# Performance work log

Measured on AMD Instinct MI355X. Metric: run time of the kernel, lower is better.

## Reference

```python
import jax, jax.numpy as jnp
import numpy as np

EMB_DIM = 2048
HIDDEN_DIM = 8192
BATCH = 4
SEQ = 2048


def _kaiming_normal(key, out_f, in_f):
    # kaiming_normal_(mode='fan_in', nonlinearity='relu'): std = sqrt(2 / fan_in)
    std = np.sqrt(2.0 / in_f).astype(np.float32)
    return jax.random.normal(key, (out_f, in_f), dtype=jnp.float32) * std


def setup_inputs() -> dict:
    key = jax.random.key(0)
    kx, k1, k2, k3 = jax.random.split(key, 4)
    x = jax.random.normal(kx, (BATCH, SEQ, EMB_DIM), dtype=jnp.float32)
    w1 = _kaiming_normal(k1, HIDDEN_DIM, EMB_DIM)   # fc1.weight [hidden, emb]
    w2 = _kaiming_normal(k2, HIDDEN_DIM, EMB_DIM)   # fc2.weight [hidden, emb]
    w3 = _kaiming_normal(k3, EMB_DIM, HIDDEN_DIM)   # fc3.weight [emb, hidden]
    return {"x": x, "w1": w1, "w2": w2, "w3": w3, "scale_x": 1}


def reference(x, w1, w2, w3, scale_x):
    # fc1/fc2: x @ W.T  (no bias). scale_x is unused in the fp (calibration) path.
    gate = jnp.einsum('bse,he->bsh', x, w1)  # [B,S,H]
    up = jnp.einsum('bse,he->bsh', x, w2)    # [B,S,H]
    h = jax.nn.silu(gate) * up               # Custom_SiLU + Custom_ElementWiseMul
    out = jnp.einsum('bsh,eh->bse', h, w3)   # fc3 down-projection
    return out
```

## Files before the change

kernel.cpp:

```cpp
#include <hip/hip_runtime.h>
#include <hip/hip_bf16.h>

#define M_ROWS 8192
#define E_DIM  2048
#define H_DIM  8192

typedef __attribute__((ext_vector_type(8))) short bf16x8;
typedef __attribute__((ext_vector_type(4))) float f32x4;
typedef __attribute__((ext_vector_type(4))) unsigned int uint4v;

__device__ __forceinline__ unsigned short f2bf_rne(float x) {
  unsigned u = __builtin_bit_cast(unsigned, x);
  u += 0x7FFFu + ((u >> 16) & 1u);
  return (unsigned short)(u >> 16);
}

__device__ __forceinline__ float bf2f(unsigned short b) {
  unsigned u = ((unsigned)b) << 16;
  return __builtin_bit_cast(float, u);
}

__global__ __launch_bounds__(256) void cvt_f32_bf16(const float* __restrict__ in,
                                                    unsigned short* __restrict__ out,
                                                    int n8) {
  int i = blockIdx.x * blockDim.x + threadIdx.x;
  if (i >= n8) return;
  const float4* p = (const float4*)(in + (size_t)i * 8);
  float4 a = p[0];
  float4 b = p[1];
  union { unsigned short us[8]; uint4v v; } r;
  r.us[0] = f2bf_rne(a.x); r.us[1] = f2bf_rne(a.y);
  r.us[2] = f2bf_rne(a.z); r.us[3] = f2bf_rne(a.w);
  r.us[4] = f2bf_rne(b.x); r.us[5] = f2bf_rne(b.y);
  r.us[6] = f2bf_rne(b.z); r.us[7] = f2bf_rne(b.w);
  *(uint4v*)(out + (size_t)i * 8) = r.v;
}

__device__ __forceinline__ void gld_lds16(const unsigned short* g, unsigned short* l) {
  __builtin_amdgcn_global_load_lds(
      (const __attribute__((address_space(1))) unsigned int*)g,
      (__attribute__((address_space(3))) unsigned int*)l, 16, 0, 0);
}

#define VMCNT(n)   asm volatile("s_waitcnt vmcnt(" #n ")" ::: "memory")

template <int EPI>
__global__ __launch_bounds__(512, 2)
void gemm256(const unsigned short* __restrict__ A,
             const unsigned short* __restrict__ B,
             const unsigned short* __restrict__ Gate,
             void* __restrict__ Cout,
             int M, int N, int K) {
  __shared__ unsigned short lA[2][16384];
  __shared__ unsigned short lB[2][16384];

  const int tid = threadIdx.x;
  const int lane = tid & 63;
  const int wave = tid >> 6;
  const int wr = wave >> 2;
  const int wc = wave & 3;
  const int lr = lane & 15, lk = lane >> 4;

  const int gx = gridDim.x;
  const int nwg = gx * gridDim.y;
  const int wg = blockIdx.y * gx + blockIdx.x;
  const int swz = (wg & 7) * (nwg >> 3) + (wg >> 3);
  const int bcol = swz % gx, brow = swz / gx;

  const unsigned short* Ag = A + (size_t)brow * 256 * K;
  const unsigned short* Bg = B + (size_t)bcol * 256 * K;

  f32x4 acc[8][4] = {};
  const int NT = K >> 6;
  const int NI = NT >> 1;

  auto stageH = [&](const unsigned short* gbase, unsigned short* ldsh) {
#pragma unroll
    for (int i = 0; i < 2; ++i) {
      int p = i * 4096 + tid * 8;
      int row = p >> 6;
      int lslot = ((p >> 3) & 7) ^ (row & 7);
      gld_lds16(gbase + (size_t)row * K + lslot * 8, ldsh + p);
    }
  };

  const int xsw = (lr & 7) << 3;
  bf16x8 af[8][2], bf[4][2];

#define RD_A(MLO, SRC) \
  _Pragma("unroll") for (int m = MLO; m < MLO + 4; ++m) { \
    int r = wr * 128 + m * 16 + lr; \
    af[m][0] = *(const bf16x8*)&SRC[(r * 64 + lk * 8) ^ xsw]; \
    af[m][1] = *(const bf16x8*)&SRC[(r * 64 + 32 + lk * 8) ^ xsw]; }
#define RD_B(NLO, SRC) \
  _Pragma("unroll") for (int n = NLO; n < NLO + 2; ++n) { \
    int r = wc * 64 + n * 16 + lr; \
    bf[n][0] = *(const bf16x8*)&SRC[(r * 64 + lk * 8) ^ xsw]; \
    bf[n][1] = *(const bf16x8*)&SRC[(r * 64 + 32 + lk * 8) ^ xsw]; }
#define PH_MFMA(MLO, NLO) \
  __builtin_amdgcn_s_barrier(); \
  asm volatile("s_waitcnt lgkmcnt(0)" ::: "memory"); \
  __builtin_amdgcn_sched_barrier(0); \
  __builtin_amdgcn_s_setprio(1); \
  _Pragma("unroll") for (int m = MLO; m < MLO + 4; ++m) \
  _Pragma("unroll") for (int n = NLO; n < NLO + 2; ++n) \
  _Pragma("unroll") for (int ks = 0; ks < 2; ++ks) \
    acc[m][n] = __builtin_amdgcn_mfma_f32_16x16x32_bf16(af[m][ks], bf[n][ks], acc[m][n], 0, 0, 0); \
  __builtin_amdgcn_s_setprio(0);

  stageH(Ag, &lA[0][0]);
  stageH(Ag + (size_t)128 * K, &lA[0][8192]);
  stageH(Bg, &lB[0][0]);
  stageH(Bg + (size_t)128 * K, &lB[0][8192]);
  stageH(Ag + 64, &lA[1][0]);
  stageH(Ag + (size_t)128 * K + 64, &lA[1][8192]);
  stageH(Bg + 64, &lB[1][0]);
  stageH(Bg + (size_t)128 * K + 64, &lB[1][8192]);
  VMCNT(0);
  __builtin_amdgcn_s_barrier();

  const unsigned short* lA0 = &lA[0][0];
  const unsigned short* lB0 = &lB[0][0];
  const unsigned short* lA1 = &lA[1][0];
  const unsigned short* lB1 = &lB[1][0];

  for (int it = 0; it < NI; ++it) {
    const int t = it << 1;
    const size_t kT1 = (size_t)(t + 1) * 64;
    const size_t kS2 = (size_t)((t + 2 < NT) ? t + 2 : NT - 1) * 64;
    const size_t kS3 = (size_t)((t + 3 < NT) ? t + 3 : NT - 1) * 64;

    RD_A(0, lA0); RD_B(0, lB0);
    if (it > 0) stageH(Ag + (size_t)128 * K + kT1, &lA[1][8192]);
    asm volatile("s_waitcnt lgkmcnt(8)" ::: "memory");
    PH_MFMA(0, 0);
    __builtin_amdgcn_s_barrier();

    RD_B(2, lB0);
    PH_MFMA(0, 2);
    __builtin_amdgcn_s_barrier();

    RD_A(4, lA0);
    stageH(Bg + kS2, &lB[0][0]);
    PH_MFMA(4, 0);
    __builtin_amdgcn_s_barrier();

    stageH(Bg + (size_t)128 * K + kS2, &lB[0][8192]);
    stageH(Ag + kS2, &lA[0][0]);
    PH_MFMA(4, 2);
    VMCNT(6);
    __builtin_amdgcn_s_barrier();

    RD_A(0, lA1); RD_B(0, lB1);
    stageH(Ag + (size_t)128 * K + kS2, &lA[0][8192]);
    asm volatile("s_waitcnt lgkmcnt(8)" ::: "memory");
    PH_MFMA(0, 0);
    __builtin_amdgcn_s_barrier();

    RD_B(2, lB1);
    PH_MFMA(0, 2);
    __builtin_amdgcn_s_barrier();

    RD_A(4, lA1);
    stageH(Bg + kS3, &lB[1][0]);
    PH_MFMA(4, 0);
    __builtin_amdgcn_s_barrier();

    stageH(Bg + (size_t)128 * K + kS3, &lB[1][8192]);
    stageH(Ag + kS3, &lA[1][0]);
    PH_MFMA(4, 2);
    VMCNT(6);
    __builtin_amdgcn_s_barrier();
  }
  VMCNT(0);

#undef RD_A
#undef RD_B
#undef PH_MFMA

  const int row0 = brow * 256 + wr * 128 + lk * 4;
  const int col0 = bcol * 256 + wc * 64 + lr;
#pragma unroll
  for (int m = 0; m < 8; ++m) {
#pragma unroll
    for (int n = 0; n < 4; ++n) {
#pragma unroll
      for (int j = 0; j < 4; ++j) {
        size_t idx = (size_t)(row0 + m * 16 + j) * N + (col0 + n * 16);
        float v = acc[m][n][j];
        if constexpr (EPI == 0) {
          ((float*)Cout)[idx] = v;
        } else if constexpr (EPI == 1) {
          ((unsigned short*)Cout)[idx] = f2bf_rne(v);
        } else {
          float g = bf2f(Gate[idx]);
          float s = g / (1.0f + __expf(-g));
          ((unsigned short*)Cout)[idx] = f2bf_rne(s * v);
        }
      }
    }
  }
}

extern "C" void kernel_launch(void* const* d_in, const int* in_sizes, int n_in,
                              void* d_out, int out_size, void* d_ws, size_t ws_size,
                              hipStream_t stream) {
  const float* x  = (const float*)d_in[0];
  const float* w1 = (const float*)d_in[1];
  const float* w2 = (const float*)d_in[2];
  const float* w3 = (const float*)d_in[3];
  float* out = (float*)d_out;

  const int M = M_ROWS, E = E_DIM, H = H_DIM;

  unsigned short* xb  = (unsigned short*)d_ws;
  unsigned short* w1b = xb + (size_t)M * E;
  unsigned short* gb  = w1b + (size_t)H * E;
  unsigned short* w2b = w1b;
  unsigned short* w3b = xb;

  const int n8 = (M * E) / 8;
  cvt_f32_bf16<<<dim3(n8 / 256), 256, 0, stream>>>(x, xb, n8);
  cvt_f32_bf16<<<dim3(n8 / 256), 256, 0, stream>>>(w1, w1b, n8);

  gemm256<1><<<dim3(H / 256, M / 256), 512, 0, stream>>>(xb, w1b, nullptr, gb, M, H, E);

  cvt_f32_bf16<<<dim3(n8 / 256), 256, 0, stream>>>(w2, w2b, n8);

  gemm256<2><<<dim3(H / 256, M / 256), 512, 0, stream>>>(xb, w2b, gb, gb, M, H, E);

  cvt_f32_bf16<<<dim3(n8 / 256), 256, 0, stream>>>(w3, w3b, n8);

  gemm256<0><<<dim3(E / 256, M / 256), 512, 0, stream>>>(gb, w3b, nullptr, out, M, E, H);
}
```

Baseline: 871.7 us.

## Switch GEMM to 32x32x16 MFMA with fragment-ordered LDS layout

Replaces the 16x16x32 bf16 MFMA tiling with 32x32x16 MFMA, so each wave computes a 4x2 grid of 32x32 subtiles. The global-to-LDS staging now writes tiles in a fragment-contiguous layout, where each 32x16 block sits as 512 contiguous elements. LDS reads then become linear per-lane loads with no XOR swizzle. The goal is fewer MFMA issues and fewer LDS reads per FLOP; the cost is a changed bank-conflict pattern and global loads that are less contiguous, with 16-element runs per row.

```diff
diff --git a/kernel.cpp b/kernel.cpp
--- a/kernel.cpp
+++ b/kernel.cpp
@@ -6,7 +6,7 @@
 #define H_DIM  8192
 
 typedef __attribute__((ext_vector_type(8))) short bf16x8;
-typedef __attribute__((ext_vector_type(4))) float f32x4;
+typedef __attribute__((ext_vector_type(16))) float f32x16;
 typedef __attribute__((ext_vector_type(4))) unsigned int uint4v;
 
 __device__ __forceinline__ unsigned short f2bf_rne(float x) {
@@ -59,7 +59,7 @@
   const int wave = tid >> 6;
   const int wr = wave >> 2;
   const int wc = wave & 3;
-  const int lr = lane & 15, lk = lane >> 4;
+  const int wr4 = wr * 4, wc2 = wc * 2;
 
   const int gx = gridDim.x;
   const int nwg = gx * gridDim.y;
@@ -70,42 +70,40 @@
   const unsigned short* Ag = A + (size_t)brow * 256 * K;
   const unsigned short* Bg = B + (size_t)bcol * 256 * K;
 
-  f32x4 acc[8][4] = {};
+  f32x16 acc[4][2] = {};
   const int NT = K >> 6;
   const int NI = NT >> 1;
 
+  const int ep0 = tid * 8, ep1 = 4096 + tid * 8;
+  size_t soff0, soff1;
+  {
+    int blk = ep0 >> 9, l = (ep0 >> 3) & 63;
+    soff0 = (size_t)((blk >> 2) * 32 + (l & 31)) * K + ((blk & 3) * 16 + ((l >> 5) << 3));
+    blk = ep1 >> 9; l = (ep1 >> 3) & 63;
+    soff1 = (size_t)((blk >> 2) * 32 + (l & 31)) * K + ((blk & 3) * 16 + ((l >> 5) << 3));
+  }
   auto stageH = [&](const unsigned short* gbase, unsigned short* ldsh) {
-#pragma unroll
-    for (int i = 0; i < 2; ++i) {
-      int p = i * 4096 + tid * 8;
-      int row = p >> 6;
-      int lslot = ((p >> 3) & 7) ^ (row & 7);
-      gld_lds16(gbase + (size_t)row * K + lslot * 8, ldsh + p);
-    }
+    gld_lds16(gbase + soff0, ldsh + ep0);
+    gld_lds16(gbase + soff1, ldsh + ep1);
   };
 
-  const int xsw = (lr & 7) << 3;
-  bf16x8 af[8][2], bf[4][2];
+  bf16x8 afr[4][4], bfr[2][4];
 
 #define RD_A(MLO, SRC) \
-  _Pragma("unroll") for (int m = MLO; m < MLO + 4; ++m) { \
-    int r = wr * 128 + m * 16 + lr; \
-    af[m][0] = *(const bf16x8*)&SRC[(r * 64 + lk * 8) ^ xsw]; \
-    af[m][1] = *(const bf16x8*)&SRC[(r * 64 + 32 + lk * 8) ^ xsw]; }
-#define RD_B(NLO, SRC) \
-  _Pragma("unroll") for (int n = NLO; n < NLO + 2; ++n) { \
-    int r = wc * 64 + n * 16 + lr; \
-    bf[n][0] = *(const bf16x8*)&SRC[(r * 64 + lk * 8) ^ xsw]; \
-    bf[n][1] = *(const bf16x8*)&SRC[(r * 64 + 32 + lk * 8) ^ xsw]; }
-#define PH_MFMA(MLO, NLO) \
+  _Pragma("unroll") for (int ms = MLO; ms < MLO + 2; ++ms) \
+  _Pragma("unroll") for (int ks = 0; ks < 4; ++ks) \
+    afr[ms][ks] = *(const bf16x8*)&SRC[(((wr4 + ms) << 2) + ks) * 512 + (lane << 3)];
+#define RD_B(NS, SRC) \
+  _Pragma("unroll") for (int ks = 0; ks < 4; ++ks) \
+    bfr[NS][ks] = *(const bf16x8*)&SRC[(((wc2 + NS) << 2) + ks) * 512 + (lane << 3)];
+#define PH_MFMA(MLO, NS) \
   __builtin_amdgcn_s_barrier(); \
   asm volatile("s_waitcnt lgkmcnt(0)" ::: "memory"); \
   __builtin_amdgcn_sched_barrier(0); \
   __builtin_amdgcn_s_setprio(1); \
-  _Pragma("unroll") for (int m = MLO; m < MLO + 4; ++m) \
-  _Pragma("unroll") for (int n = NLO; n < NLO + 2; ++n) \
-  _Pragma("unroll") for (int ks = 0; ks < 2; ++ks) \
-    acc[m][n] = __builtin_amdgcn_mfma_f32_16x16x32_bf16(af[m][ks], bf[n][ks], acc[m][n], 0, 0, 0); \
+  _Pragma("unroll") for (int ms = MLO; ms < MLO + 2; ++ms) \
+  _Pragma("unroll") for (int ks = 0; ks < 4; ++ks) \
+    acc[ms][NS] = __builtin_amdgcn_mfma_f32_32x32x16_bf16(afr[ms][ks], bfr[NS][ks], acc[ms][NS], 0, 0, 0); \
   __builtin_amdgcn_s_setprio(0);
 
   stageH(Ag, &lA[0][0]);
@@ -136,18 +134,18 @@
     PH_MFMA(0, 0);
     __builtin_amdgcn_s_barrier();
 
-    RD_B(2, lB0);
-    PH_MFMA(0, 2);
-    __builtin_amdgcn_s_barrier();
-
-    RD_A(4, lA0);
+    RD_B(1, lB0);
+    PH_MFMA(0, 1);
+    __builtin_amdgcn_s_barrier();
+
+    RD_A(2, lA0);
     stageH(Bg + kS2, &lB[0][0]);
-    PH_MFMA(4, 0);
+    PH_MFMA(2, 0);
     __builtin_amdgcn_s_barrier();
 
     stageH(Bg + (size_t)128 * K + kS2, &lB[0][8192]);
     stageH(Ag + kS2, &lA[0][0]);
-    PH_MFMA(4, 2);
+    PH_MFMA(2, 1);
     VMCNT(6);
     __builtin_amdgcn_s_barrier();
 
@@ -157,18 +155,18 @@
     PH_MFMA(0, 0);
     __builtin_amdgcn_s_barrier();
 
-    RD_B(2, lB1);
-    PH_MFMA(0, 2);
-    __builtin_amdgcn_s_barrier();
-
-    RD_A(4, lA1);
+    RD_B(1, lB1);
+    PH_MFMA(0, 1);
+    __builtin_amdgcn_s_barrier();
+
+    RD_A(2, lA1);
     stageH(Bg + kS3, &lB[1][0]);
-    PH_MFMA(4, 0);
+    PH_MFMA(2, 0);
     __builtin_amdgcn_s_barrier();
 
     stageH(Bg + (size_t)128 * K + kS3, &lB[1][8192]);
     stageH(Ag + kS3, &lA[1][0]);
-    PH_MFMA(4, 2);
+    PH_MFMA(2, 1);
     VMCNT(6);
     __builtin_amdgcn_s_barrier();
   }
@@ -178,16 +176,17 @@
 #undef RD_B
 #undef PH_MFMA
 
-  const int row0 = brow * 256 + wr * 128 + lk * 4;
-  const int col0 = bcol * 256 + wc * 64 + lr;
+  const int row0 = brow * 256 + wr * 128 + 4 * (lane >> 5);
+  const int col0 = bcol * 256 + wc * 64 + (lane & 31);
 #pragma unroll
-  for (int m = 0; m < 8; ++m) {
+  for (int ms = 0; ms < 4; ++ms) {
 #pragma unroll
-    for (int n = 0; n < 4; ++n) {
+    for (int ns = 0; ns < 2; ++ns) {
 #pragma unroll
-      for (int j = 0; j < 4; ++j) {
-        size_t idx = (size_t)(row0 + m * 16 + j) * N + (col0 + n * 16);
-        float v = acc[m][n][j];
+      for (int reg = 0; reg < 16; ++reg) {
+        int r = row0 + ms * 32 + (reg & 3) + 8 * (reg >> 2);
+        size_t idx = (size_t)r * N + (col0 + ns * 32);
+        float v = acc[ms][ns][reg];
         if constexpr (EPI == 0) {
           ((float*)Cout)[idx] = v;
         } else if constexpr (EPI == 1) {
```

Measured after the change: 1.038 ms. +19.1%, slower.

## Fuse gate and up GEMMs into one dual-B kernel with SiLU epilogue

Applied to the files above, without the earlier changes.

Each workgroup now loads 128 rows of w1 and 128 rows of w2 into the B tile, computes gate and up together, and combines them through LDS in the epilogue to write silu(gate)*up. This removes a separate GEMM pass, the round trip of the bf16 gate tensor through global memory, and the extra read of x. The three f32-to-bf16 conversions are also merged into one launch. The cost is a larger workspace (w1b, w2b and h stored separately) and an LDS-staged epilogue in which half the waves idle.

```diff
diff --git a/kernel.cpp b/kernel.cpp
--- a/kernel.cpp
+++ b/kernel.cpp
@@ -15,16 +15,14 @@
   return (unsigned short)(u >> 16);
 }
 
-__device__ __forceinline__ float bf2f(unsigned short b) {
-  unsigned u = ((unsigned)b) << 16;
-  return __builtin_bit_cast(float, u);
-}
-
-__global__ __launch_bounds__(256) void cvt_f32_bf16(const float* __restrict__ in,
-                                                    unsigned short* __restrict__ out,
-                                                    int n8) {
+__global__ __launch_bounds__(256) void cvt3_f32_bf16(const float* __restrict__ s0, unsigned short* __restrict__ d0,
+                                                     const float* __restrict__ s1, unsigned short* __restrict__ d1,
+                                                     const float* __restrict__ s2, unsigned short* __restrict__ d2,
+                                                     int n8) {
   int i = blockIdx.x * blockDim.x + threadIdx.x;
   if (i >= n8) return;
+  const float* in = (blockIdx.y == 0) ? s0 : (blockIdx.y == 1) ? s1 : s2;
+  unsigned short* out = (blockIdx.y == 0) ? d0 : (blockIdx.y == 1) ? d1 : d2;
   const float4* p = (const float4*)(in + (size_t)i * 8);
   float4 a = p[0];
   float4 b = p[1];
@@ -48,11 +46,12 @@
 __global__ __launch_bounds__(512, 2)
 void gemm256(const unsigned short* __restrict__ A,
              const unsigned short* __restrict__ B,
-             const unsigned short* __restrict__ Gate,
+             const unsigned short* __restrict__ B2,
              void* __restrict__ Cout,
              int M, int N, int K) {
-  __shared__ unsigned short lA[2][16384];
-  __shared__ unsigned short lB[2][16384];
+  __shared__ unsigned short sh[65536];
+  unsigned short* lAb = sh;
+  unsigned short* lBb = sh + 32768;
 
   const int tid = threadIdx.x;
   const int lane = tid & 63;
@@ -68,7 +67,15 @@
   const int bcol = swz % gx, brow = swz / gx;
 
   const unsigned short* Ag = A + (size_t)brow * 256 * K;
-  const unsigned short* Bg = B + (size_t)bcol * 256 * K;
+  const unsigned short* BgH0;
+  const unsigned short* BgH1;
+  if constexpr (EPI == 3) {
+    BgH0 = B  + (size_t)bcol * 128 * K;
+    BgH1 = B2 + (size_t)bcol * 128 * K;
+  } else {
+    BgH0 = B + (size_t)bcol * 256 * K;
+    BgH1 = BgH0 + (size_t)128 * K;
+  }
 
   f32x4 acc[8][4] = {};
   const int NT = K >> 6;
@@ -108,21 +115,21 @@
     acc[m][n] = __builtin_amdgcn_mfma_f32_16x16x32_bf16(af[m][ks], bf[n][ks], acc[m][n], 0, 0, 0); \
   __builtin_amdgcn_s_setprio(0);
 
-  stageH(Ag, &lA[0][0]);
-  stageH(Ag + (size_t)128 * K, &lA[0][8192]);
-  stageH(Bg, &lB[0][0]);
-  stageH(Bg + (size_t)128 * K, &lB[0][8192]);
-  stageH(Ag + 64, &lA[1][0]);
-  stageH(Ag + (size_t)128 * K + 64, &lA[1][8192]);
-  stageH(Bg + 64, &lB[1][0]);
-  stageH(Bg + (size_t)128 * K + 64, &lB[1][8192]);
+  stageH(Ag, lAb);
+  stageH(Ag + (size_t)128 * K, lAb + 8192);
+  stageH(BgH0, lBb);
+  stageH(BgH1, lBb + 8192);
+  stageH(Ag + 64, lAb + 16384);
+  stageH(Ag + (size_t)128 * K + 64, lAb + 16384 + 8192);
+  stageH(BgH0 + 64, lBb + 16384);
+  stageH(BgH1 + 64, lBb + 16384 + 8192);
   VMCNT(0);
   __builtin_amdgcn_s_barrier();
 
-  const unsigned short* lA0 = &lA[0][0];
-  const unsigned short* lB0 = &lB[0][0];
-  const unsigned short* lA1 = &lA[1][0];
-  const unsigned short* lB1 = &lB[1][0];
+  const unsigned short* lA0 = lAb;
+  const unsigned short* lB0 = lBb;
+  const unsigned short* lA1 = lAb + 16384;
+  const unsigned short* lB1 = lBb + 16384;
 
   for (int it = 0; it < NI; ++it) {
     const int t = it << 1;
@@ -131,7 +138,7 @@
     const size_t kS3 = (size_t)((t + 3 < NT) ? t + 3 : NT - 1) * 64;
 
     RD_A(0, lA0); RD_B(0, lB0);
-    if (it > 0) stageH(Ag + (size_t)128 * K + kT1, &lA[1][8192]);
+    if (it > 0) stageH(Ag + (size_t)128 * K + kT1, lAb + 16384 + 8192);
     asm volatile("s_waitcnt lgkmcnt(8)" ::: "memory");
     PH_MFMA(0, 0);
     __builtin_amdgcn_s_barrier();
@@ -141,18 +148,18 @@
     __builtin_amdgcn_s_barrier();
 
     RD_A(4, lA0);
-    stageH(Bg + kS2, &lB[0][0]);
+    stageH(BgH0 + kS2, lBb);
     PH_MFMA(4, 0);
     __builtin_amdgcn_s_barrier();
 
-    stageH(Bg + (size_t)128 * K + kS2, &lB[0][8192]);
-    stageH(Ag + kS2, &lA[0][0]);
+    stageH(BgH1 + kS2, lBb + 8192);
+    stageH(Ag + kS2, lAb);
     PH_MFMA(4, 2);
     VMCNT(6);
     __builtin_amdgcn_s_barrier();
 
     RD_A(0, lA1); RD_B(0, lB1);
-    stageH(Ag + (size_t)128 * K + kS2, &lA[0][8192]);
+    stageH(Ag + (size_t)128 * K + kS2, lAb + 8192);
     asm volatile("s_waitcnt lgkmcnt(8)" ::: "memory");
     PH_MFMA(0, 0);
     __builtin_amdgcn_s_barrier();
@@ -162,12 +169,12 @@
     __builtin_amdgcn_s_barrier();
 
     RD_A(4, lA1);
-    stageH(Bg + kS3, &lB[1][0]);
+    stageH(BgH0 + kS3, lBb + 16384);
     PH_MFMA(4, 0);
     __builtin_amdgcn_s_barrier();
 
-    stageH(Bg + (size_t)128 * K + kS3, &lB[1][8192]);
-    stageH(Ag + kS3, &lA[1][0]);
+    stageH(BgH1 + kS3, lBb + 16384 + 8192);
+    stageH(Ag + kS3, lAb + 16384);
     PH_MFMA(4, 2);
     VMCNT(6);
     __builtin_amdgcn_s_barrier();
@@ -178,27 +185,49 @@
 #undef RD_B
 #undef PH_MFMA
 
-  const int row0 = brow * 256 + wr * 128 + lk * 4;
-  const int col0 = bcol * 256 + wc * 64 + lr;
-#pragma unroll
-  for (int m = 0; m < 8; ++m) {
-#pragma unroll
-    for (int n = 0; n < 4; ++n) {
-#pragma unroll
-      for (int j = 0; j < 4; ++j) {
-        size_t idx = (size_t)(row0 + m * 16 + j) * N + (col0 + n * 16);
-        float v = acc[m][n][j];
-        if constexpr (EPI == 0) {
-          ((float*)Cout)[idx] = v;
-        } else if constexpr (EPI == 1) {
-          ((unsigned short*)Cout)[idx] = f2bf_rne(v);
-        } else {
-          float g = bf2f(Gate[idx]);
-          float s = g / (1.0f + __expf(-g));
-          ((unsigned short*)Cout)[idx] = f2bf_rne(s * v);
+  if constexpr (EPI == 3) {
+    __builtin_amdgcn_s_barrier();
+    if (wc >= 2) {
+      float* rg = (float*)(sh + (wr * 2 + (wc - 2)) * 16384);
+#pragma unroll
+      for (int m = 0; m < 8; ++m)
+#pragma unroll
+        for (int n = 0; n < 4; ++n)
+#pragma unroll
+          for (int j = 0; j < 4; ++j)
+            rg[(m * 16 + n * 4 + j) * 64 + lane] = acc[m][n][j];
+    }
+    asm volatile("s_waitcnt lgkmcnt(0)" ::: "memory");
+    __builtin_amdgcn_s_barrier();
+    if (wc < 2) {
+      const float* rg = (const float*)(sh + (wr * 2 + wc) * 16384);
+      const int row0 = brow * 256 + wr * 128 + lk * 4;
+      const int col0 = bcol * 128 + wc * 64 + lr;
+#pragma unroll
+      for (int m = 0; m < 8; ++m)
+#pragma unroll
+        for (int n = 0; n < 4; ++n)
+#pragma unroll
+          for (int j = 0; j < 4; ++j) {
+            float g = acc[m][n][j];
+            float u = rg[(m * 16 + n * 4 + j) * 64 + lane];
+            float s = g / (1.0f + __expf(-g));
+            ((unsigned short*)Cout)[(size_t)(row0 + m * 16 + j) * N + (col0 + n * 16)] =
+                f2bf_rne(s * u);
+          }
+    }
+  } else {
+    const int row0 = brow * 256 + wr * 128 + lk * 4;
+    const int col0 = bcol * 256 + wc * 64 + lr;
+#pragma unroll
+    for (int m = 0; m < 8; ++m)
+#pragma unroll
+      for (int n = 0; n < 4; ++n)
+#pragma unroll
+        for (int j = 0; j < 4; ++j) {
+          size_t idx = (size_t)(row0 + m * 16 + j) * N + (col0 + n * 16);
+          ((float*)Cout)[idx] = acc[m][n][j];
         }
-      }
-    }
   }
 }
 
@@ -215,21 +244,16 @@
 
   unsigned short* xb  = (unsigned short*)d_ws;
   unsigned short* w1b = xb + (size_t)M * E;
-  unsigned short* gb  = w1b + (size_t)H * E;
-  unsigned short* w2b = w1b;
+  unsigned short* w2b = w1b + (size_t)H * E;
+  unsigned short* hb  = w2b + (size_t)H * E;
   unsigned short* w3b = xb;
 
   const int n8 = (M * E) / 8;
-  cvt_f32_bf16<<<dim3(n8 / 256), 256, 0, stream>>>(x, xb, n8);
-  cvt_f32_bf16<<<dim3(n8 / 256), 256, 0, stream>>>(w1, w1b, n8);
-
-  gemm256<1><<<dim3(H / 256, M / 256), 512, 0, stream>>>(xb, w1b, nullptr, gb, M, H, E);
-
-  cvt_f32_bf16<<<dim3(n8 / 256), 256, 0, stream>>>(w2, w2b, n8);
-
-  gemm256<2><<<dim3(H / 256, M / 256), 512, 0, stream>>>(xb, w2b, gb, gb, M, H, E);
-
-  cvt_f32_bf16<<<dim3(n8 / 256), 256, 0, stream>>>(w3, w3b, n8);
-
-  gemm256<0><<<dim3(E / 256, M / 256), 512, 0, stream>>>(gb, w3b, nullptr, out, M, E, H);
-}
+  cvt3_f32_bf16<<<dim3(n8 / 256, 3), 256, 0, stream>>>(x, xb, w1, w1b, w2, w2b, n8);
+
+  gemm256<3><<<dim3(H / 128, M / 256), 512, 0, stream>>>(xb, w1b, w2b, hb, M, H, E);
+
+  cvt3_f32_bf16<<<dim3(n8 / 256, 1), 256, 0, stream>>>(w3, w3b, w3, w3b, w3, w3b, n8);
+
+  gemm256<0><<<dim3(E / 256, M / 256), 512, 0, stream>>>(hb, w3b, nullptr, out, M, E, H);
+}
```

Result: faster. 832.5 us (-4.5%).
